# Optimization experiments

Hardware: AMD Instinct MI355X
Metric: run time of the kernel (lower is better)

The kernel has to match this reference:

```python
import jax, jax.numpy as jnp
import numpy as np

B = 4096          # batch
N_REPS = 16       # number of irreducible reps (all same d here)
N_ELEMS = 128     # group elements per rep
D = 32            # block dimension
N_SYMBOLS = 64    # alphabet size
EMB = N_REPS * D * D  # 16384


def setup_inputs() -> dict:
    key = jax.random.key(0)
    k1, k2, k3, k4 = jax.random.split(key, 4)
    state_embedding = jax.random.normal(k1, (B, EMB), dtype=jnp.float32)
    input_symbols = jax.random.randint(k2, (B,), 0, N_SYMBOLS, dtype=jnp.int64)
    reps = jax.random.normal(k3, (N_REPS, N_ELEMS, D, D), dtype=jnp.float32)
    transitions = jax.random.randint(k4, (N_SYMBOLS,), 0, N_ELEMS, dtype=jnp.int64)
    return {"state_embedding": state_embedding, "input_symbols": input_symbols,
            "reps": reps, "transitions": transitions}


def reference(state_embedding, input_symbols, reps, transitions):
    # state_embedding: [B, n_reps*d*d]; reps: [n_reps, n_elems, d, d]
    n_reps, n_elems, d, _ = reps.shape
    b = state_embedding.shape[0]
    # Split embedding into block-diagonal d x d blocks (all reps same d).
    blocks = jnp.nan_to_num(state_embedding.reshape(b, n_reps, d, d))  # [b, r, d, d]
    # Per-symbol gather: symbol -> group element -> rep matrix.
    t = transitions[input_symbols]            # [b]
    M = jnp.nan_to_num(reps[:, t])            # [r, b, d, d]
    # Per-matrix Frobenius normalization (matches rep_matrix.norm()).
    fro = jnp.sqrt(jnp.sum(M * M, axis=(-2, -1), keepdims=True))
    M = M / (fro + 1e-6)
    # Block-diagonal batched matmul: block @ rep_matrix per (batch, rep).
    out = jnp.einsum('brij,rbjk->brik', blocks, M)  # [b, r, d, d]
    return out.reshape(b, -1)
```

## Files before the change

### kernel.cpp

```cpp
#include <hip/hip_runtime.h>

#define NREPS   16
#define NELEMS  128
#define DD      32
#define MATSZ   (DD * DD)
#define EMB     (NREPS * MATSZ)

__global__ __launch_bounds__(256) void trans_fused_kernel(
    const float* __restrict__ emb,
    const int*   __restrict__ syms,
    const float* __restrict__ reps,
    const int*   __restrict__ trans,
    float*       __restrict__ out)
{
    __shared__ float lA[4 * MATSZ];
    __shared__ float lM[4 * MATSZ];
    const int bid = blockIdx.x;
    const int b   = bid >> 2;
    const int w   = threadIdx.x >> 6;
    const int l   = threadIdx.x & 63;
    const int r   = ((bid & 3) << 2) | w;

    const int esym = trans[syms[b]];

    const float4* Ag = reinterpret_cast<const float4*>(
        emb + (size_t)b * EMB + (size_t)r * MATSZ);
    const float4* Mg = reinterpret_cast<const float4*>(
        reps + ((size_t)r * NELEMS + esym) * MATSZ);
    float4* lwA = reinterpret_cast<float4*>(lA + w * MATSZ);
    float4* lwM = reinterpret_cast<float4*>(lM + w * MATSZ);

    #pragma unroll
    for (int it = 0; it < 4; ++it) {
        const int f4 = it * 64 + l;
        const int i  = f4 >> 3;
        const int k4 = f4 & 7;
        lwA[i * 8 + (k4 ^ ((i >> 2) & 7))] = Ag[f4];
        lwM[f4] = Mg[f4];
    }

    const int i0 = (l >> 3) << 2;
    const int j0 = (l & 7);
    const int sw = (l >> 3) & 7;

    float acc[4][4];
    #pragma unroll
    for (int m = 0; m < 4; ++m)
        #pragma unroll
        for (int j = 0; j < 4; ++j) acc[m][j] = 0.0f;

    float ss = 0.0f;

    #pragma unroll
    for (int kb = 0; kb < 8; ++kb) {
        float4 a[4];
        #pragma unroll
        for (int m = 0; m < 4; ++m)
            a[m] = lwA[(i0 + m) * 8 + (kb ^ sw)];

        float4 mv[4];
        #pragma unroll
        for (int kk = 0; kk < 4; ++kk)
            mv[kk] = lwM[(kb * 4 + kk) * 8 + j0];

        #pragma unroll
        for (int kk = 0; kk < 4; ++kk) {
            ss += mv[kk].x * mv[kk].x + mv[kk].y * mv[kk].y
                + mv[kk].z * mv[kk].z + mv[kk].w * mv[kk].w;
            #pragma unroll
            for (int m = 0; m < 4; ++m) {
                const float av = (&a[m].x)[kk];
                acc[m][0] += av * mv[kk].x;
                acc[m][1] += av * mv[kk].y;
                acc[m][2] += av * mv[kk].z;
                acc[m][3] += av * mv[kk].w;
            }
        }
    }

    ss += __shfl_xor(ss, 1, 64);
    ss += __shfl_xor(ss, 2, 64);
    ss += __shfl_xor(ss, 4, 64);
    const float scale = 1.0f / (sqrtf(ss) + 1e-6f);

    float* Ob = out + (size_t)b * EMB + (size_t)r * MATSZ + i0 * DD + j0 * 4;
    #pragma unroll
    for (int m = 0; m < 4; ++m) {
        float4 o = make_float4(acc[m][0] * scale, acc[m][1] * scale,
                               acc[m][2] * scale, acc[m][3] * scale);
        *reinterpret_cast<float4*>(Ob + m * DD) = o;
    }
}

extern "C" void kernel_launch(void* const* d_in, const int* in_sizes, int n_in,
                              void* d_out, int out_size, void* d_ws, size_t ws_size,
                              hipStream_t stream) {
    const float* emb   = (const float*)d_in[0];
    const int*   syms  = (const int*)d_in[1];
    const float* reps  = (const float*)d_in[2];
    const int*   trans = (const int*)d_in[3];
    float* outp = (float*)d_out;

    const int B = in_sizes[1];

    hipLaunchKernelGGL(trans_fused_kernel, dim3(B * 4), dim3(256), 0, stream,
                       emb, syms, reps, trans, outp);
}
```

Measured before the change: 124.9 us.

## Process four reps per wave with register-prefetched double buffering

Each block now handles a whole batch row, and each wave loops over four reps instead of one, cutting the grid to a quarter of its former size. While computing the current rep's matmul from LDS, the wave prefetches the next rep's blocks into registers, then writes them to LDS after compute. The Frobenius sum now comes from the global load data with a full-wave reduction instead of being recomputed inside the inner loop. This trades fewer blocks and lower latency hiding from occupancy for software pipelining and higher register pressure.

Measured after the change: 121.5 us. 2.8% less time.

```diff
diff --git a/kernel.cpp b/kernel.cpp
--- a/kernel.cpp
+++ b/kernel.cpp
@@ -15,80 +15,111 @@
 {
     __shared__ float lA[4 * MATSZ];
     __shared__ float lM[4 * MATSZ];
-    const int bid = blockIdx.x;
-    const int b   = bid >> 2;
-    const int w   = threadIdx.x >> 6;
-    const int l   = threadIdx.x & 63;
-    const int r   = ((bid & 3) << 2) | w;
+    const int b = blockIdx.x;
+    const int w = threadIdx.x >> 6;
+    const int l = threadIdx.x & 63;
 
     const int esym = trans[syms[b]];
 
-    const float4* Ag = reinterpret_cast<const float4*>(
-        emb + (size_t)b * EMB + (size_t)r * MATSZ);
-    const float4* Mg = reinterpret_cast<const float4*>(
-        reps + ((size_t)r * NELEMS + esym) * MATSZ);
     float4* lwA = reinterpret_cast<float4*>(lA + w * MATSZ);
     float4* lwM = reinterpret_cast<float4*>(lM + w * MATSZ);
 
+    const int i0 = (l >> 3) << 2;
+    const int j0 = l & 7;
+    const int sw = (l >> 3) & 7;
+
+    float4 ra[4], rm[4];
+
+    {
+        const float4* Ag = reinterpret_cast<const float4*>(
+            emb + (size_t)b * EMB + (size_t)(w * 4) * MATSZ);
+        const float4* Mg = reinterpret_cast<const float4*>(
+            reps + ((size_t)(w * 4) * NELEMS + esym) * MATSZ);
+        #pragma unroll
+        for (int it = 0; it < 4; ++it) { ra[it] = Ag[it * 64 + l]; rm[it] = Mg[it * 64 + l]; }
+    }
+    float ss_cur = 0.0f, ss_nxt = 0.0f;
     #pragma unroll
     for (int it = 0; it < 4; ++it) {
         const int f4 = it * 64 + l;
-        const int i  = f4 >> 3;
-        const int k4 = f4 & 7;
-        lwA[i * 8 + (k4 ^ ((i >> 2) & 7))] = Ag[f4];
-        lwM[f4] = Mg[f4];
+        const int i = f4 >> 3, k4 = f4 & 7;
+        lwA[i * 8 + (k4 ^ ((i >> 2) & 7))] = ra[it];
+        lwM[f4] = rm[it];
+        ss_cur += rm[it].x * rm[it].x + rm[it].y * rm[it].y
+                + rm[it].z * rm[it].z + rm[it].w * rm[it].w;
     }
 
-    const int i0 = (l >> 3) << 2;
-    const int j0 = (l & 7);
-    const int sw = (l >> 3) & 7;
+    #pragma unroll
+    for (int p = 0; p < 4; ++p) {
+        const int r = w * 4 + p;
 
-    float acc[4][4];
-    #pragma unroll
-    for (int m = 0; m < 4; ++m)
-        #pragma unroll
-        for (int j = 0; j < 4; ++j) acc[m][j] = 0.0f;
+        if (p < 3) {
+            const float4* Ag = reinterpret_cast<const float4*>(
+                emb + (size_t)b * EMB + (size_t)(r + 1) * MATSZ);
+            const float4* Mg = reinterpret_cast<const float4*>(
+                reps + ((size_t)(r + 1) * NELEMS + esym) * MATSZ);
+            #pragma unroll
+            for (int it = 0; it < 4; ++it) { ra[it] = Ag[it * 64 + l]; rm[it] = Mg[it * 64 + l]; }
+        }
 
-    float ss = 0.0f;
-
-    #pragma unroll
-    for (int kb = 0; kb < 8; ++kb) {
-        float4 a[4];
+        float acc[4][4];
         #pragma unroll
         for (int m = 0; m < 4; ++m)
-            a[m] = lwA[(i0 + m) * 8 + (kb ^ sw)];
-
-        float4 mv[4];
-        #pragma unroll
-        for (int kk = 0; kk < 4; ++kk)
-            mv[kk] = lwM[(kb * 4 + kk) * 8 + j0];
+            #pragma unroll
+            for (int j = 0; j < 4; ++j) acc[m][j] = 0.0f;
 
         #pragma unroll
-        for (int kk = 0; kk < 4; ++kk) {
-            ss += mv[kk].x * mv[kk].x + mv[kk].y * mv[kk].y
-                + mv[kk].z * mv[kk].z + mv[kk].w * mv[kk].w;
+        for (int kb = 0; kb < 8; ++kb) {
+            float4 a[4];
             #pragma unroll
-            for (int m = 0; m < 4; ++m) {
-                const float av = (&a[m].x)[kk];
-                acc[m][0] += av * mv[kk].x;
-                acc[m][1] += av * mv[kk].y;
-                acc[m][2] += av * mv[kk].z;
-                acc[m][3] += av * mv[kk].w;
+            for (int m = 0; m < 4; ++m)
+                a[m] = lwA[(i0 + m) * 8 + (kb ^ sw)];
+            float4 mv[4];
+            #pragma unroll
+            for (int kk = 0; kk < 4; ++kk)
+                mv[kk] = lwM[(kb * 4 + kk) * 8 + j0];
+            #pragma unroll
+            for (int kk = 0; kk < 4; ++kk)
+                #pragma unroll
+                for (int m = 0; m < 4; ++m) {
+                    const float av = (&a[m].x)[kk];
+                    acc[m][0] += av * mv[kk].x;
+                    acc[m][1] += av * mv[kk].y;
+                    acc[m][2] += av * mv[kk].z;
+                    acc[m][3] += av * mv[kk].w;
+                }
+        }
+
+        if (p < 3) {
+            ss_nxt = 0.0f;
+            #pragma unroll
+            for (int it = 0; it < 4; ++it) {
+                const int f4 = it * 64 + l;
+                const int i = f4 >> 3, k4 = f4 & 7;
+                lwA[i * 8 + (k4 ^ ((i >> 2) & 7))] = ra[it];
+                lwM[f4] = rm[it];
+                ss_nxt += rm[it].x * rm[it].x + rm[it].y * rm[it].y
+                        + rm[it].z * rm[it].z + rm[it].w * rm[it].w;
             }
         }
-    }
 
-    ss += __shfl_xor(ss, 1, 64);
-    ss += __shfl_xor(ss, 2, 64);
-    ss += __shfl_xor(ss, 4, 64);
-    const float scale = 1.0f / (sqrtf(ss) + 1e-6f);
+        float ss = ss_cur;
+        ss += __shfl_xor(ss, 1, 64);
+        ss += __shfl_xor(ss, 2, 64);
+        ss += __shfl_xor(ss, 4, 64);
+        ss += __shfl_xor(ss, 8, 64);
+        ss += __shfl_xor(ss, 16, 64);
+        ss += __shfl_xor(ss, 32, 64);
+        const float scale = 1.0f / (sqrtf(ss) + 1e-6f);
 
-    float* Ob = out + (size_t)b * EMB + (size_t)r * MATSZ + i0 * DD + j0 * 4;
-    #pragma unroll
-    for (int m = 0; m < 4; ++m) {
-        float4 o = make_float4(acc[m][0] * scale, acc[m][1] * scale,
-                               acc[m][2] * scale, acc[m][3] * scale);
-        *reinterpret_cast<float4*>(Ob + m * DD) = o;
+        float* Ob = out + (size_t)b * EMB + (size_t)r * MATSZ + i0 * DD + j0 * 4;
+        #pragma unroll
+        for (int m = 0; m < 4; ++m) {
+            float4 o = make_float4(acc[m][0] * scale, acc[m][1] * scale,
+                                   acc[m][2] * scale, acc[m][3] * scale);
+            *reinterpret_cast<float4*>(Ob + m * DD) = o;
+        }
+        ss_cur = ss_nxt;
     }
 }
 
@@ -103,6 +134,6 @@
 
     const int B = in_sizes[1];
 
-    hipLaunchKernelGGL(trans_fused_kernel, dim3(B * 4), dim3(256), 0, stream,
+    hipLaunchKernelGGL(trans_fused_kernel, dim3(B), dim3(256), 0, stream,
                        emb, syms, reps, trans, outp);
 }
```
